# Kernel tuning notes

Measured on AMD Instinct MI355X. Metric: run time of the kernel, lower is better.

The kernel has to match this reference:

```python
import jax, jax.numpy as jnp
import numpy as np

B, S, C, L = 4, 32, 256, 512
H = 8
D = L // H  # head_size = 64
EPS = 1e-5


def _layernorm(x, g, b):
    mu = jnp.mean(x, axis=-1, keepdims=True)
    var = jnp.var(x, axis=-1, keepdims=True)
    return (x - mu) * jax.lax.rsqrt(var + EPS) * g + b


def setup_inputs() -> dict:
    key = jax.random.key(0)
    ks = jax.random.split(key, 12)
    s = 1.0 / np.sqrt(L)
    return {
        "x": jax.random.normal(ks[0], (B, S, C, L), dtype=jnp.float32),
        # per-head QKV weights, stacked: [H, D, L] (torch Linear(L, D, bias=False).weight)
        "Wq": jax.random.normal(ks[1], (H, D, L), dtype=jnp.float32) * s,
        "Wk": jax.random.normal(ks[2], (H, D, L), dtype=jnp.float32) * s,
        "Wv": jax.random.normal(ks[3], (H, D, L), dtype=jnp.float32) * s,
        # output projection Linear(L, L)
        "Wo": jax.random.normal(ks[4], (L, L), dtype=jnp.float32) * s,
        "bo": jnp.zeros((L,), dtype=jnp.float32),
        # FFN Linear(L, 4L) -> ReLU -> Linear(4L, L)
        "W1": jax.random.normal(ks[5], (4 * L, L), dtype=jnp.float32) * s,
        "b1": jnp.zeros((4 * L,), dtype=jnp.float32),
        "W2": jax.random.normal(ks[6], (L, 4 * L), dtype=jnp.float32) * (1.0 / np.sqrt(4 * L)),
        "b2": jnp.zeros((L,), dtype=jnp.float32),
        # LayerNorm params
        "g1": jnp.ones((L,), dtype=jnp.float32),
        "be1": jnp.zeros((L,), dtype=jnp.float32),
        "g2": jnp.ones((L,), dtype=jnp.float32),
        "be2": jnp.zeros((L,), dtype=jnp.float32),
    }


def reference(x, Wq, Wk, Wv, Wo, bo, W1, b1, W2, b2, g1, be1, g2, be2):
    # --- regional multi-head self-attention (pre-LN, residual) ---
    h = _layernorm(x, g1, be1)                        # [B,S,C,L]
    q = jnp.einsum('bscl,hdl->bhscd', h, Wq)          # [B,H,S,C,D]
    k = jnp.einsum('bscl,hdl->bhscd', h, Wk)
    v = jnp.einsum('bscl,hdl->bhscd', h, Wv)
    wei = jnp.einsum('bhsqd,bhskd->bhsqk', q, k) * (D ** -0.5)  # [B,H,S,C,C]
    wei = jax.nn.softmax(wei, axis=-1)                # no causal mask (tril unused)
    out = jnp.einsum('bhsqk,bhskd->bhsqd', wei, v)    # [B,H,S,C,D]
    out = jnp.transpose(out, (0, 2, 3, 1, 4)).reshape(x.shape[0], x.shape[1], x.shape[2], H * D)
    out = out @ Wo.T + bo                             # proj Linear(L, L)
    x = x + out
    # --- feed-forward (pre-LN, residual) ---
    h2 = _layernorm(x, g2, be2)
    ff = jax.nn.relu(h2 @ W1.T + b1) @ W2.T + b2      # [B,S,C,L]
    return x + ff
```

## Files before the change

kernel.cpp:

```cpp
#include <hip/hip_runtime.h>
#include <cstdint>
#include <cstddef>

#define NTOK 32768
#define LDIM 512
#define HN 8
#define HD 64
#define CC 256
#define FFD 2048

typedef __bf16 bf16x8 __attribute__((ext_vector_type(8)));
typedef float f32x4 __attribute__((ext_vector_type(4)));
typedef unsigned short u16;
typedef unsigned int u32;

__device__ __forceinline__ u16 f2bf(float f) {
  u32 u = __float_as_uint(f);
  u32 r = (u + 0x7fffu + ((u >> 16) & 1u)) >> 16;
  return (u16)r;
}

__device__ __forceinline__ void gload_lds16(const void* g, void* l) {
  __builtin_amdgcn_global_load_lds(
      (__attribute__((address_space(1))) void*)(void*)g,
      (__attribute__((address_space(3))) void*)l, 16, 0, 0);
}

__global__ void k_convall(const float* __restrict__ Wq, const float* __restrict__ Wk,
                          const float* __restrict__ Wv, const float* __restrict__ Wo,
                          const float* __restrict__ W1, const float* __restrict__ W2,
                          u16* __restrict__ wqkv, u16* __restrict__ wo,
                          u16* __restrict__ w1, u16* __restrict__ w2) {
  const int NW = 262144;
  const int MW = 1048576;
  const int TOT = 4 * NW + 2 * MW;
  int i = blockIdx.x * blockDim.x + threadIdx.x;
  const int st = gridDim.x * blockDim.x;
  for (; i < TOT; i += st) {
    if (i < NW) wqkv[i] = f2bf(Wq[i]);
    else if (i < 2 * NW) wqkv[i] = f2bf(Wk[i - NW]);
    else if (i < 3 * NW) wqkv[i] = f2bf(Wv[i - 2 * NW]);
    else if (i < 4 * NW) wo[i - 3 * NW] = f2bf(Wo[i - 3 * NW]);
    else if (i < 4 * NW + MW) w1[i - 4 * NW] = f2bf(W1[i - 4 * NW]);
    else w2[i - 4 * NW - MW] = f2bf(W2[i - 4 * NW - MW]);
  }
}

__global__ __launch_bounds__(256) void k_ln(const float* __restrict__ x,
                                            const float* __restrict__ gam,
                                            const float* __restrict__ bet,
                                            u16* __restrict__ out) {
  const int row = blockIdx.x * 4 + (threadIdx.x >> 6);
  const int lane = threadIdx.x & 63;
  const float4* xr = (const float4*)(x + (size_t)row * LDIM);
  float4 a = xr[lane * 2], b = xr[lane * 2 + 1];
  float s = a.x + a.y + a.z + a.w + b.x + b.y + b.z + b.w;
  float q = a.x * a.x + a.y * a.y + a.z * a.z + a.w * a.w +
            b.x * b.x + b.y * b.y + b.z * b.z + b.w * b.w;
#pragma unroll
  for (int m = 1; m < 64; m <<= 1) { s += __shfl_xor(s, m); q += __shfl_xor(q, m); }
  const float mean = s * (1.f / LDIM);
  const float rs = rsqrtf(q * (1.f / LDIM) - mean * mean + 1e-5f);
  const int c0 = lane * 8;
  const float4* g4 = (const float4*)(gam + c0);
  const float4* b4 = (const float4*)(bet + c0);
  float4 ga = g4[0], gb = g4[1], ba = b4[0], bb = b4[1];
  float vin[8] = {a.x, a.y, a.z, a.w, b.x, b.y, b.z, b.w};
  float vg[8]  = {ga.x, ga.y, ga.z, ga.w, gb.x, gb.y, gb.z, gb.w};
  float vb[8]  = {ba.x, ba.y, ba.z, ba.w, bb.x, bb.y, bb.z, bb.w};
  u16 o[8];
#pragma unroll
  for (int i = 0; i < 8; ++i) o[i] = f2bf((vin[i] - mean) * rs * vg[i] + vb[i]);
  *(bf16x8*)(out + (size_t)row * LDIM + c0) = *(bf16x8*)o;
}


__device__ __forceinline__ void stage_half(const u16* __restrict__ g, int K,
                                           u16* __restrict__ lds, int t) {
#pragma unroll
  for (int i = 0; i < 2; ++i) {
    const int p = i * 512 + t;
    const int r = p >> 2;
    const int c = ((p & 3) ^ ((r >> 1) & 3)) << 3;
    gload_lds16(g + (size_t)r * K + c, lds + ((i * 512 + (t & ~63)) << 3));
  }
}

__device__ __forceinline__ bf16x8 ldsfrag(const u16* __restrict__ s, int R, int kq) {
  return *(const bf16x8*)(s + R * 32 + ((kq ^ ((R >> 1) & 3)) << 3));
}

#define VM6 asm volatile("s_waitcnt vmcnt(6)" ::: "memory")
#define VM4 asm volatile("s_waitcnt vmcnt(4)" ::: "memory")
#define VM0 asm volatile("s_waitcnt vmcnt(0)" ::: "memory")
#define LGKM0 asm volatile("s_waitcnt lgkmcnt(0)" ::: "memory")
#define BARRIER asm volatile("s_barrier" ::: "memory")

template <int EPI>
__global__ __launch_bounds__(512, 2) void k_gemm8(const u16* __restrict__ A,
                                                  const u16* __restrict__ Bw, int K,
                                                  const float* __restrict__ bias,
                                                  const float* __restrict__ resid,
                                                  void* __restrict__ outp, int ldc,
                                                  int bmN) {
  extern __shared__ u16 lds_g[];
  const int t = threadIdx.x;
  const int lane = t & 63;
  const int w = t >> 6;
  const int wm = w >> 2, wn = w & 3;
  const int rl = lane & 15;
  const int kq = lane >> 4;
  const int nwg = gridDim.x;
  const int cpx = nwg >> 3;
  const int id = blockIdx.x;
  const int sid = (id & 7) * cpx + (id >> 3);
  const int bm = sid % bmN, bn = sid / bmN;

  const u16* Ag = A + (size_t)bm * 256 * K;
  const u16* Bg = Bw + (size_t)bn * 256 * K;
  u16* SA0 = lds_g;
  u16* SB0 = lds_g + 32768;
#define SA(par, kh) (SA0 + (par) * 16384 + (kh) * 8192)
#define SB(par, kh) (SB0 + (par) * 16384 + (kh) * 8192)

  f32x4 acc[8][4] = {};

  stage_half(Ag, K, SA(0, 0), t);
  stage_half(Bg, K, SB(0, 0), t);
  stage_half(Ag + 32, K, SA(0, 1), t);
  stage_half(Bg + 32, K, SB(0, 1), t);

  const int NT = K >> 6;
  const int rA = wm * 128 + rl;
  const int rB = wn * 64 + rl;

#define MFMA16(ACCBASE)                                                          \
  LGKM0;                                                                         \
  __builtin_amdgcn_sched_barrier(0);                                             \
  __builtin_amdgcn_s_setprio(1);                                                 \
  _Pragma("unroll") for (int f = 0; f < 4; ++f)                                  \
      _Pragma("unroll") for (int n = 0; n < 4; ++n)                              \
          acc[(ACCBASE) + f][n] =                                                \
              __builtin_amdgcn_mfma_f32_16x16x32_bf16(a[f], b[n],                \
                                                      acc[(ACCBASE) + f][n],     \
                                                      0, 0, 0);                  \
  __builtin_amdgcn_s_setprio(0)

  for (int T = 0; T < NT; ++T) {
    const int par = T & 1, nx = par ^ 1;
    const u16* An = Ag + (size_t)(T + 1) * 64;
    const u16* Bn = Bg + (size_t)(T + 1) * 64;
    const bool hn = (T + 1 < NT);
    bf16x8 a[4], b[4];
    {
      if (hn) { stage_half(An, K, SA(nx, 0), t); VM6; } else { VM4; }
      BARRIER;
      const u16* s = SA(par, 0);
#pragma unroll
      for (int f = 0; f < 4; ++f) a[f] = ldsfrag(s, rA + f * 16, kq);
      const u16* sb = SB(par, 0);
#pragma unroll
      for (int n = 0; n < 4; ++n) b[n] = ldsfrag(sb, rB + n * 16, kq);
      MFMA16(0);
    }
    {
      if (hn) stage_half(Bn, K, SB(nx, 0), t);
      BARRIER;
      const u16* s = SA(par, 0);
#pragma unroll
      for (int f = 0; f < 4; ++f) a[f] = ldsfrag(s, rA + 64 + f * 16, kq);
      MFMA16(4);
    }
    {
      if (hn) { stage_half(An + 32, K, SA(nx, 1), t); VM6; } else { VM0; }
      BARRIER;
      const u16* s = SA(par, 1);
#pragma unroll
      for (int f = 0; f < 4; ++f) a[f] = ldsfrag(s, rA + f * 16, kq);
      const u16* sb = SB(par, 1);
#pragma unroll
      for (int n = 0; n < 4; ++n) b[n] = ldsfrag(sb, rB + n * 16, kq);
      MFMA16(0);
    }
    {
      if (hn) stage_half(Bn + 32, K, SB(nx, 1), t);
      BARRIER;
      const u16* s = SA(par, 1);
#pragma unroll
      for (int f = 0; f < 4; ++f) a[f] = ldsfrag(s, rA + 64 + f * 16, kq);
      MFMA16(4);
    }
  }
#undef SA
#undef SB
#undef MFMA16

  const int rg = (lane >> 4) * 4;
  const int cl = lane & 15;
#pragma unroll
  for (int mi = 0; mi < 8; ++mi)
#pragma unroll
    for (int n = 0; n < 4; ++n) {
      const int mg = bm * 256 + wm * 128 + mi * 16 + rg;
      const int og = bn * 256 + wn * 64 + n * 16 + cl;
#pragma unroll
      for (int r = 0; r < 4; ++r) {
        float v = acc[mi][n][r];
        size_t idx = (size_t)(mg + r) * ldc + og;
        if (EPI == 0) {
          ((u16*)outp)[idx] = f2bf(v);
        } else if (EPI == 1) {
          ((float*)outp)[idx] = resid[idx] + v + bias[og];
        } else if (EPI == 2) {
          ((u16*)outp)[idx] = f2bf(fmaxf(v + bias[og], 0.f));
        } else {
          ((float*)outp)[idx] = ((float*)outp)[idx] + v + bias[og];
        }
      }
    }
}

__device__ __forceinline__ int swz(int row, int col) {
  return row * 64 + (col ^ ((row & 7) << 3));
}

__global__ __launch_bounds__(256) void k_attn(const u16* __restrict__ qkv,
                                              u16* __restrict__ attn) {
  __shared__ u16 Ks[64 * 64];
  __shared__ u16 Vt[64 * 64];
  __shared__ u16 Pl[4 * 64 * 64];
  const int t = threadIdx.x, lane = t & 63, w = t >> 6;
  const int region = blockIdx.x >> 3;
  const int h = blockIdx.x & 7;
  const size_t n0 = (size_t)region * CC;
  const int qb = w * 64;
  const int rl = lane & 15;
  const int kg = (lane >> 4) * 8;
  u16* Pw = Pl + w * 4096;

  bf16x8 aq[4][2];
#pragma unroll
  for (int f = 0; f < 4; ++f)
#pragma unroll
    for (int ks = 0; ks < 2; ++ks)
      aq[f][ks] = *(const bf16x8*)&qkv[(n0 + qb + f * 16 + rl) * 1536 + h * 64 + ks * 32 + kg];

  f32x4 oacc[4][4] = {};
  float mrun[4][4], lrun[4][4];
#pragma unroll
  for (int i = 0; i < 4; ++i)
#pragma unroll
    for (int j = 0; j < 4; ++j) { mrun[i][j] = -1e30f; lrun[i][j] = 0.f; }

  const int sr = t >> 2;
  const int sc = (t & 3) * 16;
  for (int kt = 0; kt < 4; ++kt) {
    if (kt) __syncthreads();
    {
      const u16* kp = &qkv[(n0 + kt * 64 + sr) * 1536 + 512 + h * 64 + sc];
      bf16x8 k0 = *(const bf16x8*)kp;
      bf16x8 k1 = *(const bf16x8*)(kp + 8);
      *(bf16x8*)&Ks[swz(sr, sc)] = k0;
      *(bf16x8*)&Ks[swz(sr, sc + 8)] = k1;
      const u16* vp = &qkv[(n0 + kt * 64 + sr) * 1536 + 1024 + h * 64 + sc];
      bf16x8 v0 = *(const bf16x8*)vp;
      bf16x8 v1 = *(const bf16x8*)(vp + 8);
#pragma unroll
      for (int i = 0; i < 8; ++i) Vt[swz(sc + i, sr)] = ((u16*)&v0)[i];
#pragma unroll
      for (int i = 0; i < 8; ++i) Vt[swz(sc + 8 + i, sr)] = ((u16*)&v1)[i];
    }
    __syncthreads();
    f32x4 sacc[4][4] = {};
#pragma unroll
    for (int ks = 0; ks < 2; ++ks) {
      bf16x8 bk[4];
#pragma unroll
      for (int f = 0; f < 4; ++f) bk[f] = *(const bf16x8*)&Ks[swz(f * 16 + rl, ks * 32 + kg)];
#pragma unroll
      for (int i = 0; i < 4; ++i)
#pragma unroll
        for (int j = 0; j < 4; ++j)
          sacc[i][j] = __builtin_amdgcn_mfma_f32_16x16x32_bf16(aq[i][ks], bk[j], sacc[i][j], 0, 0, 0);
    }
#pragma unroll
    for (int i = 0; i < 4; ++i)
#pragma unroll
      for (int j = 0; j < 4; ++j)
#pragma unroll
        for (int r = 0; r < 4; ++r) sacc[i][j][r] *= 0.125f;
#pragma unroll
    for (int i = 0; i < 4; ++i) {
#pragma unroll
      for (int r = 0; r < 4; ++r) {
        float v = fmaxf(fmaxf(sacc[i][0][r], sacc[i][1][r]), fmaxf(sacc[i][2][r], sacc[i][3][r]));
#pragma unroll
        for (int m = 1; m < 16; m <<= 1) v = fmaxf(v, __shfl_xor(v, m));
        float mnew = fmaxf(mrun[i][r], v);
        float fac = __expf(mrun[i][r] - mnew);
        mrun[i][r] = mnew;
        float ps = 0.f;
#pragma unroll
        for (int fn = 0; fn < 4; ++fn) {
          float p = __expf(sacc[i][fn][r] - mnew);
          sacc[i][fn][r] = p;
          ps += p;
        }
#pragma unroll
        for (int m = 1; m < 16; m <<= 1) ps += __shfl_xor(ps, m);
        lrun[i][r] = lrun[i][r] * fac + ps;
#pragma unroll
        for (int fd = 0; fd < 4; ++fd) oacc[i][fd][r] *= fac;
      }
#pragma unroll
      for (int fn = 0; fn < 4; ++fn)
#pragma unroll
        for (int r = 0; r < 4; ++r)
          Pw[swz(i * 16 + (lane >> 4) * 4 + r, fn * 16 + rl)] = f2bf(sacc[i][fn][r]);
    }
#pragma unroll
    for (int ks = 0; ks < 2; ++ks) {
      bf16x8 ap[4], bv[4];
#pragma unroll
      for (int f = 0; f < 4; ++f) ap[f] = *(const bf16x8*)&Pw[swz(f * 16 + rl, ks * 32 + kg)];
#pragma unroll
      for (int f = 0; f < 4; ++f) bv[f] = *(const bf16x8*)&Vt[swz(f * 16 + rl, ks * 32 + kg)];
#pragma unroll
      for (int i = 0; i < 4; ++i)
#pragma unroll
        for (int j = 0; j < 4; ++j)
          oacc[i][j] = __builtin_amdgcn_mfma_f32_16x16x32_bf16(ap[i], bv[j], oacc[i][j], 0, 0, 0);
    }
  }
#pragma unroll
  for (int i = 0; i < 4; ++i)
#pragma unroll
    for (int fd = 0; fd < 4; ++fd)
#pragma unroll
      for (int r = 0; r < 4; ++r) {
        float v = oacc[i][fd][r] / lrun[i][r];
        attn[(n0 + qb + i * 16 + (lane >> 4) * 4 + r) * 512 + h * 64 + fd * 16 + rl] = f2bf(v);
      }
}

extern "C" void kernel_launch(void* const* d_in, const int* in_sizes, int n_in,
                              void* d_out, int out_size, void* d_ws, size_t ws_size,
                              hipStream_t stream) {
  (void)in_sizes; (void)n_in; (void)out_size; (void)ws_size;
  const float* x   = (const float*)d_in[0];
  const float* Wq  = (const float*)d_in[1];
  const float* Wk  = (const float*)d_in[2];
  const float* Wv  = (const float*)d_in[3];
  const float* Wo  = (const float*)d_in[4];
  const float* bo  = (const float*)d_in[5];
  const float* W1  = (const float*)d_in[6];
  const float* b1  = (const float*)d_in[7];
  const float* W2  = (const float*)d_in[8];
  const float* b2  = (const float*)d_in[9];
  const float* g1  = (const float*)d_in[10];
  const float* be1 = (const float*)d_in[11];
  const float* g2  = (const float*)d_in[12];
  const float* be2 = (const float*)d_in[13];
  float* out = (float*)d_out;

  char* ws = (char*)d_ws;
  u16* wqkv = (u16*)(ws + 0);
  u16* wo   = (u16*)(ws + 1572864);
  u16* w1   = (u16*)(ws + 2097152);
  u16* w2   = (u16*)(ws + 4194304);
  u16* regA = (u16*)(ws + 6291456);
  u16* regB = (u16*)(ws + 39845888);

  const size_t LDSB = 131072;

  k_convall<<<1024, 256, 0, stream>>>(Wq, Wk, Wv, Wo, W1, W2, wqkv, wo, w1, w2);
  k_ln<<<NTOK / 4, 256, 0, stream>>>(x, g1, be1, regA);
  k_gemm8<0><<<dim3(128 * 6), 512, LDSB, stream>>>(regA, wqkv, 512, nullptr, nullptr, regB, 1536, 128);
  k_attn<<<dim3(4 * 32 * 8), 256, 0, stream>>>(regB, regA);
  k_gemm8<1><<<dim3(128 * 2), 512, LDSB, stream>>>(regA, wo, 512, bo, x, out, 512, 128);
  k_ln<<<NTOK / 4, 256, 0, stream>>>(out, g2, be2, regA);
  k_gemm8<2><<<dim3(128 * 8), 512, LDSB, stream>>>(regA, w1, 512, b1, nullptr, regB, 2048, 128);
  k_gemm8<3><<<dim3(128 * 2), 512, LDSB, stream>>>(regB, w2, 2048, b2, nullptr, out, 512, 128);
}
```

Measured before the change: 462.2 us.

## Restructure GEMM mainloop to full-K64 row-half LDS tiles with four-phase pipeline

The GEMM main loop no longer stages 32-wide K halves. It stages 128-row by 64-K tiles with an 8-way XOR swizzle, and each warp reads only the A and B halves it needs. Each K64 tile is split into four phases over row groups. Next-tile global-to-LDS loads are issued in the first two phases, and a single vmcnt(0) wait sits at the end. The goal is fewer barriers per K-step, wider LDS fragments and better overlap, at the cost of a coarser wait that may expose load latency.

```diff
diff --git a/kernel.cpp b/kernel.cpp
--- a/kernel.cpp
+++ b/kernel.cpp
@@ -75,23 +75,21 @@
 }
 
 
-__device__ __forceinline__ void stage_half(const u16* __restrict__ g, int K,
-                                           u16* __restrict__ lds, int t) {
+__device__ __forceinline__ void stage_half128(const u16* __restrict__ g, int K,
+                                              u16* __restrict__ lds, int t) {
 #pragma unroll
   for (int i = 0; i < 2; ++i) {
     const int p = i * 512 + t;
-    const int r = p >> 2;
-    const int c = ((p & 3) ^ ((r >> 1) & 3)) << 3;
+    const int r = p >> 3;
+    const int c = ((p & 7) ^ (r & 7)) << 3;
     gload_lds16(g + (size_t)r * K + c, lds + ((i * 512 + (t & ~63)) << 3));
   }
 }
 
-__device__ __forceinline__ bf16x8 ldsfrag(const u16* __restrict__ s, int R, int kq) {
-  return *(const bf16x8*)(s + R * 32 + ((kq ^ ((R >> 1) & 3)) << 3));
-}
-
-#define VM6 asm volatile("s_waitcnt vmcnt(6)" ::: "memory")
-#define VM4 asm volatile("s_waitcnt vmcnt(4)" ::: "memory")
+__device__ __forceinline__ bf16x8 ldsfrag64(const u16* __restrict__ s, int R, int ck) {
+  return *(const bf16x8*)(s + R * 64 + ((ck ^ (R & 7)) << 3));
+}
+
 #define VM0 asm volatile("s_waitcnt vmcnt(0)" ::: "memory")
 #define LGKM0 asm volatile("s_waitcnt lgkmcnt(0)" ::: "memory")
 #define BARRIER asm volatile("s_barrier" ::: "memory")
@@ -118,82 +116,68 @@
 
   const u16* Ag = A + (size_t)bm * 256 * K;
   const u16* Bg = Bw + (size_t)bn * 256 * K;
-  u16* SA0 = lds_g;
-  u16* SB0 = lds_g + 32768;
-#define SA(par, kh) (SA0 + (par) * 16384 + (kh) * 8192)
-#define SB(par, kh) (SB0 + (par) * 16384 + (kh) * 8192)
+  u16* const SAm = lds_g + (wm ? 16384 : 0);
+  u16* const SBm = lds_g + 32768 + ((wn >> 1) ? 16384 : 0);
+  const int rBl = (wn & 1) * 64;
 
   f32x4 acc[8][4] = {};
 
-  stage_half(Ag, K, SA(0, 0), t);
-  stage_half(Bg, K, SB(0, 0), t);
-  stage_half(Ag + 32, K, SA(0, 1), t);
-  stage_half(Bg + 32, K, SB(0, 1), t);
+  stage_half128(Ag, K, lds_g + 0, t);
+  stage_half128(Ag + (size_t)128 * K, K, lds_g + 16384, t);
+  stage_half128(Bg, K, lds_g + 32768, t);
+  stage_half128(Bg + (size_t)128 * K, K, lds_g + 49152, t);
+  VM0;
+  BARRIER;
 
   const int NT = K >> 6;
-  const int rA = wm * 128 + rl;
-  const int rB = wn * 64 + rl;
-
-#define MFMA16(ACCBASE)                                                          \
-  LGKM0;                                                                         \
-  __builtin_amdgcn_sched_barrier(0);                                             \
-  __builtin_amdgcn_s_setprio(1);                                                 \
-  _Pragma("unroll") for (int f = 0; f < 4; ++f)                                  \
-      _Pragma("unroll") for (int n = 0; n < 4; ++n)                              \
-          acc[(ACCBASE) + f][n] =                                                \
-              __builtin_amdgcn_mfma_f32_16x16x32_bf16(a[f], b[n],                \
-                                                      acc[(ACCBASE) + f][n],     \
-                                                      0, 0, 0);                  \
-  __builtin_amdgcn_s_setprio(0)
-
   for (int T = 0; T < NT; ++T) {
     const int par = T & 1, nx = par ^ 1;
+    const bool hn = (T + 1 < NT);
     const u16* An = Ag + (size_t)(T + 1) * 64;
     const u16* Bn = Bg + (size_t)(T + 1) * 64;
-    const bool hn = (T + 1 < NT);
-    bf16x8 a[4], b[4];
-    {
-      if (hn) { stage_half(An, K, SA(nx, 0), t); VM6; } else { VM4; }
+    bf16x8 b[4][2];
+#pragma unroll
+    for (int p = 0; p < 4; ++p) {
+      bf16x8 a[2][2];
+#pragma unroll
+      for (int rf = 0; rf < 2; ++rf)
+#pragma unroll
+        for (int kk = 0; kk < 2; ++kk)
+          a[rf][kk] = ldsfrag64(SAm + par * 8192, p * 32 + rf * 16 + rl, kk * 4 + kq);
+      if (p == 0) {
+#pragma unroll
+        for (int n = 0; n < 4; ++n)
+#pragma unroll
+          for (int kk = 0; kk < 2; ++kk)
+            b[n][kk] = ldsfrag64(SBm + par * 8192, rBl + n * 16 + rl, kk * 4 + kq);
+        if (hn) {
+          stage_half128(An, K, lds_g + nx * 8192, t);
+          stage_half128(Bn, K, lds_g + 32768 + nx * 8192, t);
+        }
+      } else if (p == 1) {
+        if (hn) {
+          stage_half128(An + (size_t)128 * K, K, lds_g + 16384 + nx * 8192, t);
+          stage_half128(Bn + (size_t)128 * K, K, lds_g + 49152 + nx * 8192, t);
+        }
+      }
       BARRIER;
-      const u16* s = SA(par, 0);
-#pragma unroll
-      for (int f = 0; f < 4; ++f) a[f] = ldsfrag(s, rA + f * 16, kq);
-      const u16* sb = SB(par, 0);
-#pragma unroll
-      for (int n = 0; n < 4; ++n) b[n] = ldsfrag(sb, rB + n * 16, kq);
-      MFMA16(0);
-    }
-    {
-      if (hn) stage_half(Bn, K, SB(nx, 0), t);
+      LGKM0;
+      __builtin_amdgcn_sched_barrier(0);
+      __builtin_amdgcn_s_setprio(1);
+#pragma unroll
+      for (int rf = 0; rf < 2; ++rf)
+#pragma unroll
+        for (int n = 0; n < 4; ++n) {
+          acc[p * 2 + rf][n] =
+              __builtin_amdgcn_mfma_f32_16x16x32_bf16(a[rf][0], b[n][0], acc[p * 2 + rf][n], 0, 0, 0);
+          acc[p * 2 + rf][n] =
+              __builtin_amdgcn_mfma_f32_16x16x32_bf16(a[rf][1], b[n][1], acc[p * 2 + rf][n], 0, 0, 0);
+        }
+      __builtin_amdgcn_s_setprio(0);
+      if (p == 3) VM0;
       BARRIER;
-      const u16* s = SA(par, 0);
-#pragma unroll
-      for (int f = 0; f < 4; ++f) a[f] = ldsfrag(s, rA + 64 + f * 16, kq);
-      MFMA16(4);
-    }
-    {
-      if (hn) { stage_half(An + 32, K, SA(nx, 1), t); VM6; } else { VM0; }
-      BARRIER;
-      const u16* s = SA(par, 1);
-#pragma unroll
-      for (int f = 0; f < 4; ++f) a[f] = ldsfrag(s, rA + f * 16, kq);
-      const u16* sb = SB(par, 1);
-#pragma unroll
-      for (int n = 0; n < 4; ++n) b[n] = ldsfrag(sb, rB + n * 16, kq);
-      MFMA16(0);
-    }
-    {
-      if (hn) stage_half(Bn + 32, K, SB(nx, 1), t);
-      BARRIER;
-      const u16* s = SA(par, 1);
-#pragma unroll
-      for (int f = 0; f < 4; ++f) a[f] = ldsfrag(s, rA + 64 + f * 16, kq);
-      MFMA16(4);
     }
   }
-#undef SA
-#undef SB
-#undef MFMA16
 
   const int rg = (lane >> 4) * 4;
   const int cl = lane & 15;
```

After: 448.1 us. 1.03x faster.
